# Optimization experiments

Hardware: AMD Instinct MI355X
Metric: run time of the kernel (lower is better)

## Reference

```python
import jax, jax.numpy as jnp
import numpy as np

C = 64
OUT_Z = 32
HW = 128
NUM_HEADS = 4
COMP = 16          # max(c//reduction, num_heads) = 64//4
HEAD_DIM = COMP // NUM_HEADS
MAX_Z = 32
GROWTH = 16
NEG_SLOPE = 0.2


def setup_inputs() -> dict:
    key = jax.random.key(0)
    ks = jax.random.split(key, 16)
    ch = OUT_Z * C  # 2048

    def nrm(k, shape, std):
        return (jax.random.normal(k, shape, jnp.float32) * std).astype(jnp.float32)

    inp = {
        "trans_feature": jax.random.normal(ks[0], (1, ch, HW, HW), jnp.float32),
        "ln_w": jnp.ones((C,), jnp.float32),
        "ln_b": jnp.zeros((C,), jnp.float32),
        "wq": nrm(ks[1], (C, COMP), 0.05), "bq": jnp.zeros((COMP,), jnp.float32),
        "wk": nrm(ks[2], (C, COMP), 0.05), "bk": jnp.zeros((COMP,), jnp.float32),
        "wv": nrm(ks[3], (C, COMP), 0.05), "bv": jnp.zeros((COMP,), jnp.float32),
        "wo": nrm(ks[4], (COMP, C), 0.05), "bo": jnp.zeros((C,), jnp.float32),
        "rel_z_bias": nrm(ks[5], (NUM_HEADS, 2 * MAX_Z + 1), 0.02),
        "attn_gamma": jnp.asarray(0.1, jnp.float32),
        "dw0": nrm(ks[6], (ch + 0 * GROWTH, GROWTH), 0.02), "db0": jnp.zeros((GROWTH,), jnp.float32),
        "dw1": nrm(ks[7], (ch + 1 * GROWTH, GROWTH), 0.02), "db1": jnp.zeros((GROWTH,), jnp.float32),
        "dw2": nrm(ks[8], (ch + 2 * GROWTH, GROWTH), 0.02), "db2": jnp.zeros((GROWTH,), jnp.float32),
        "fuse_w": nrm(ks[9], (ch + 3 * GROWTH, ch), 0.02), "fuse_b": jnp.zeros((ch,), jnp.float32),
        "rdc_scale": jnp.asarray(0.1, jnp.float32),
        "out_z": OUT_Z,
    }
    return inp


def _conv1x1(x, w, b):
    # 1x1 conv == per-pixel dense: x [B,Cin,H,W], w [Cin,Cout]
    return jnp.einsum('bchw,co->bohw', x, w) + b[None, :, None, None]


def _lrelu(x):
    return jnp.where(x >= 0, x, NEG_SLOPE * x)


def reference(trans_feature, ln_w, ln_b, wq, bq, wk, bk, wv, bv, wo, bo,
              rel_z_bias, attn_gamma, dw0, db0, dw1, db1, dw2, db2,
              fuse_w, fuse_b, rdc_scale, out_z):
    B, Ct, H, W = trans_feature.shape
    c = Ct // out_z
    # ---- ZAxisAttention on slices [out_z, c, H, W] ----
    x = trans_feature.reshape(out_z, c, H, W)
    xf = x.transpose(0, 2, 3, 1).reshape(out_z, H * W, c)   # [Z, N, c]
    mu = xf.mean(-1, keepdims=True)
    var = ((xf - mu) ** 2).mean(-1, keepdims=True)
    normed = (xf - mu) * jax.lax.rsqrt(var + 1e-5) * ln_w + ln_b
    pooled = normed.mean(1)                                  # [Z, c]
    q = (pooled @ wq + bq).reshape(out_z, NUM_HEADS, HEAD_DIM).transpose(1, 0, 2)
    k = (pooled @ wk + bk).reshape(out_z, NUM_HEADS, HEAD_DIM).transpose(1, 0, 2)
    v = (pooled @ wv + bv).reshape(out_z, NUM_HEADS, HEAD_DIM).transpose(1, 0, 2)
    attn = jnp.einsum('hid,hjd->hij', q, k) * (HEAD_DIM ** -0.5)  # [h, Z, Z]
    zr = jnp.arange(out_z)
    rel_idx = jnp.clip(zr[None, :] - zr[:, None] + MAX_Z, 0, 2 * MAX_Z)
    attn = jax.nn.softmax(attn + rel_z_bias[:, rel_idx], axis=-1)
    o = jnp.einsum('hij,hjd->hid', attn, v).transpose(1, 0, 2).reshape(out_z, COMP)
    o = o @ wo + bo                                          # [Z, c]
    x_z = (x + attn_gamma * o[:, :, None, None]).reshape(B, Ct, H, W)
    # ---- ResidualDenseBlock on full [B, Ct, H, W] (out_z == max_out_z) ----
    feats = trans_feature
    f0 = _lrelu(_conv1x1(feats, dw0, db0))
    feats = jnp.concatenate([feats, f0], axis=1)
    f1 = _lrelu(_conv1x1(feats, dw1, db1))
    feats = jnp.concatenate([feats, f1], axis=1)
    f2 = _lrelu(_conv1x1(feats, dw2, db2))
    feats = jnp.concatenate([feats, f2], axis=1)
    fused = _lrelu(_conv1x1(feats, fuse_w, fuse_b))
    x_rdc = trans_feature + rdc_scale * fused
    return x_z + x_rdc - trans_feature
```

## Files before the change

kernel.cpp:

```cpp
#include <hip/hip_runtime.h>
#include <hip/hip_fp8.h>

typedef unsigned char u8;
typedef unsigned short u16;
typedef long lng2 __attribute__((ext_vector_type(2)));
typedef float f32x4 __attribute__((ext_vector_type(4)));
typedef u16 u16x8 __attribute__((ext_vector_type(8)));
typedef u8 u8x16 __attribute__((ext_vector_type(16)));

#define HW_N 16384
#define NCH  2048

__device__ __forceinline__ u16 f2bf(float f) {
  union { float f; unsigned u; } v; v.f = f;
  unsigned r = v.u + 0x7FFFu + ((v.u >> 16) & 1u);
  return (u16)(r >> 16);
}
__device__ __forceinline__ float bf2f(u16 u) {
  union { unsigned u; float f; } v; v.u = ((unsigned)u) << 16; return v.f;
}
__device__ __forceinline__ u8 f2fp8(float f) {
  __hip_fp8_e4m3 t(f);
  return (u8)t.__x;
}
__device__ __forceinline__ float lrelu(float v) { return v >= 0.0f ? v : 0.2f * v; }

__device__ __forceinline__ void gload_lds16(const u8* g, u8* l) {
  __builtin_amdgcn_global_load_lds((const __attribute__((address_space(1))) void*)g,
                                   (__attribute__((address_space(3))) void*)l, 16, 0, 0);
}

__global__ __launch_bounds__(256) void k_stats(const float* __restrict__ trans,
                                               u8* __restrict__ A8,
                                               float* __restrict__ pooled_sum) {
  const int z = blockIdx.x;
  const int tid = threadIdx.x;
  const int ptile = blockIdx.y;
  const int p = ptile * 256 + tid;
  const float* src = trans + (size_t)z * 64 * HW_N + p;
  float x[64];
#pragma unroll
  for (int c = 0; c < 64; ++c) x[c] = src[(size_t)c * HW_N];
  float sum = 0.f, sq = 0.f;
#pragma unroll
  for (int c = 0; c < 64; ++c) { sum += x[c]; sq += x[c] * x[c]; }
  const float mu = sum * (1.0f / 64.0f);
  const float var = sq * (1.0f / 64.0f) - mu * mu;
  const float rstd = rsqrtf(var + 1e-5f);

  __shared__ __align__(16) u8 rawt[256 * 64];
  __shared__ __align__(16) u16 normt[256 * 64];
  const int r3m = tid & 3, r7 = tid & 7;
#pragma unroll
  for (int c = 0; c < 4; ++c) {
    u8x16 y;
#pragma unroll
    for (int w = 0; w < 16; ++w) {
      const int k = (w < 8) ? (c * 8 + w) : (32 + c * 8 + (w - 8));
      y[w] = f2fp8(x[k]);
    }
    *(u8x16*)&rawt[tid * 64 + ((c ^ r3m) << 4)] = y;
  }
#pragma unroll
  for (int c8 = 0; c8 < 8; ++c8) {
    u16x8 wn;
#pragma unroll
    for (int e = 0; e < 8; ++e) wn[e] = f2bf((x[c8 * 8 + e] - mu) * rstd);
    *(u16x8*)&normt[tid * 64 + ((c8 ^ r7) << 3)] = wn;
  }
  __syncthreads();

  u8* gbase = A8 + ((size_t)z * HW_N + (size_t)ptile * 256) * 64;
#pragma unroll
  for (int it = 0; it < 4; ++it) {
    const int o = it * 256 + tid;
    const int row = o >> 2, c4 = o & 3;
    *(u8x16*)(gbase + o * 16) = *(const u8x16*)&rawt[row * 64 + ((c4 ^ (row & 3)) << 4)];
  }

  const int c = tid & 63, q = tid >> 6;
  const int kc2 = c >> 3, e2 = c & 7;
  float s = 0.f;
#pragma unroll 8
  for (int i = 0; i < 64; ++i) {
    const int row = q * 64 + i;
    s += bf2f(normt[row * 64 + ((kc2 ^ (row & 7)) << 3) + e2]);
  }
  __shared__ float red2[4][64];
  red2[q][c] = s;
  __syncthreads();
  if (tid < 64) {
    atomicAdd(&pooled_sum[z * 64 + tid],
              red2[0][tid] + red2[1][tid] + red2[2][tid] + red2[3][tid]);
  }
}

__global__ __launch_bounds__(256) void k_wdense(const float* __restrict__ dw0,
                                                const float* __restrict__ dw1,
                                                const float* __restrict__ dw2,
                                                u8* __restrict__ Wd8) {
  const int kc = blockIdx.x;
  __shared__ float tile[64][49];
  for (int idx = threadIdx.x; idx < 3072; idx += 256) {
    const int kk = idx / 48, j = idx % 48;
    const int k = kc * 64 + kk;
    float v = (j < 16) ? dw0[k * 16 + j]
            : (j < 32) ? dw1[k * 16 + (j - 16)]
                       : dw2[k * 16 + (j - 32)];
    tile[kk][j] = v;
  }
  __syncthreads();
  for (int idx = threadIdx.x; idx < 3072; idx += 256) {
    const int j = idx / 64, kk = idx % 64;
    const int pos = ((kk >> 3) & 3) * 16 + (kk & 7) + ((kk >> 5) << 3);
    Wd8[((size_t)kc * 48 + j) * 64 + pos] = f2fp8(16.0f * tile[kk][j]);
  }
}

__global__ __launch_bounds__(256) void k_dgemm(const u8* __restrict__ A8,
                                               const u8* __restrict__ Wd8,
                                               float* __restrict__ G_part) {
  __shared__ __align__(16) u8 lsA[128 * 64];
  __shared__ __align__(16) u8 lsW[48 * 64];
  const int tid = threadIdx.x;
  const int lane = tid & 63;
  const int wave = __builtin_amdgcn_readfirstlane(tid >> 6);
  const int mb = blockIdx.x;
  const int ks = blockIdx.y;
  const int r16 = lane & 15, kgrp = lane >> 4;
  const int sgoff8 = ((lane >> 2) << 6) + (((lane & 3) ^ ((lane >> 3) & 3)) << 4);
  const int kx = (kgrp ^ ((r16 >> 1) & 3)) << 4;
  f32x4 acc[3][2] = {};

  for (int t = 0; t < 16; ++t) {
    const int kc = ks * 16 + t;
    const u8* slabA = A8 + ((size_t)kc * HW_N + (size_t)mb * 128) * 64;
    const u8* slabW = Wd8 + (size_t)kc * 48 * 64;
#pragma unroll
    for (int p = 0; p < 2; ++p)
      gload_lds16(slabA + (p * 4 + wave) * 1024 + sgoff8, lsA + (p * 4 + wave) * 1024);
    if (wave < 3)
      gload_lds16(slabW + wave * 1024 + sgoff8, lsW + wave * 1024);
    asm volatile("s_waitcnt vmcnt(0)" ::: "memory");
    __syncthreads();

    lng2 wf[3], af[2];
#pragma unroll
    for (int f = 0; f < 3; ++f)
      wf[f] = *(const lng2*)(lsW + (f * 16 + r16) * 64 + kx);
#pragma unroll
    for (int g = 0; g < 2; ++g)
      af[g] = *(const lng2*)(lsA + (wave * 32 + g * 16 + r16) * 64 + kx);
#pragma unroll
    for (int f = 0; f < 3; ++f)
#pragma unroll
      for (int g = 0; g < 2; ++g) {
        acc[f][g] = __builtin_amdgcn_mfma_f32_16x16x32_fp8_fp8(wf[f][0], af[g][0], acc[f][g], 0, 0, 0);
        acc[f][g] = __builtin_amdgcn_mfma_f32_16x16x32_fp8_fp8(wf[f][1], af[g][1], acc[f][g], 0, 0, 0);
      }
    __syncthreads();
  }

  const int rg = lane >> 4;
  float* gp = G_part + (size_t)ks * 48 * HW_N;
#pragma unroll
  for (int f = 0; f < 3; ++f)
#pragma unroll
    for (int r = 0; r < 4; ++r) {
      const int j = f * 16 + rg * 4 + r;
#pragma unroll
      for (int g = 0; g < 2; ++g) {
        const int pix = mb * 128 + wave * 32 + g * 16 + r16;
        gp[(size_t)j * HW_N + pix] = acc[f][g][r] * 0.0625f;
      }
    }
}

__global__ __launch_bounds__(256) void k_dfin(const float* __restrict__ G_part,
    const float* __restrict__ dw1, const float* __restrict__ dw2,
    const float* __restrict__ db0, const float* __restrict__ db1,
    const float* __restrict__ db2, u8* __restrict__ A8) {
  const int tid = threadIdx.x;
  const int pix = blockIdx.x * 256 + tid;
  __shared__ float w1t[16][16];
  __shared__ float w2t[32][16];
  __shared__ float biases[48];
  if (tid < 256) w1t[tid >> 4][tid & 15] = dw1[(2048 + (tid >> 4)) * 16 + (tid & 15)];
  for (int idx = tid; idx < 512; idx += 256)
    w2t[idx >> 4][idx & 15] = dw2[(2048 + (idx >> 4)) * 16 + (idx & 15)];
  if (tid < 48) biases[tid] = (tid < 16) ? db0[tid] : (tid < 32) ? db1[tid - 16] : db2[tid - 32];
  __syncthreads();

  float g[48];
#pragma unroll
  for (int j = 0; j < 48; ++j)
    g[j] = G_part[(size_t)j * HW_N + pix] + G_part[(size_t)(48 + j) * HW_N + pix];

  float f0[16], f1[16], f2[16];
#pragma unroll
  for (int j = 0; j < 16; ++j) f0[j] = lrelu(g[j] + biases[j]);
#pragma unroll
  for (int j = 0; j < 16; ++j) {
    float a = g[16 + j] + biases[16 + j];
#pragma unroll
    for (int i = 0; i < 16; ++i) a += f0[i] * w1t[i][j];
    f1[j] = lrelu(a);
  }
#pragma unroll
  for (int j = 0; j < 16; ++j) {
    float a = g[32 + j] + biases[32 + j];
#pragma unroll
    for (int i = 0; i < 16; ++i) a += f0[i] * w2t[i][j];
#pragma unroll
    for (int i = 0; i < 16; ++i) a += f1[i] * w2t[16 + i][j];
    f2[j] = lrelu(a);
  }
  u8* dst = A8 + ((size_t)32 * HW_N + pix) * 64;
#pragma unroll
  for (int c = 0; c < 4; ++c) {
    u8x16 y;
#pragma unroll
    for (int w = 0; w < 16; ++w) {
      const int k = (w < 8) ? (c * 8 + w) : (32 + c * 8 + (w - 8));
      const float v = (k < 16) ? f0[k] : (k < 32) ? f1[k - 16] : (k < 48) ? f2[k - 32] : 0.0f;
      y[w] = f2fp8(v);
    }
    *(u8x16*)(dst + c * 16) = y;
  }
}

__global__ __launch_bounds__(256) void k_attn(const float* __restrict__ pooled_sum,
    const float* __restrict__ ln_w, const float* __restrict__ ln_b,
    const float* __restrict__ wq, const float* __restrict__ bq,
    const float* __restrict__ wk, const float* __restrict__ bk,
    const float* __restrict__ wv, const float* __restrict__ bv,
    const float* __restrict__ wo, const float* __restrict__ bo,
    const float* __restrict__ relz, const float* __restrict__ attn_gamma,
    float* __restrict__ o_scaled) {
  __shared__ float pooled[2048];
  __shared__ float q[512], k[512], v[512], att[4096], tz[512];
  const int tid = threadIdx.x;
  for (int i = tid; i < 2048; i += 256) {
    int c = i & 63;
    pooled[i] = ln_w[c] * pooled_sum[i] * (1.0f / 16384.0f) + ln_b[c];
  }
  __syncthreads();
  for (int i = tid; i < 512; i += 256) {
    int z = i >> 4, e = i & 15;
    float aq = bq[e], ak = bk[e], av = bv[e];
    for (int c = 0; c < 64; ++c) {
      float p = pooled[z * 64 + c];
      aq += p * wq[c * 16 + e]; ak += p * wk[c * 16 + e]; av += p * wv[c * 16 + e];
    }
    q[i] = aq; k[i] = ak; v[i] = av;
  }
  __syncthreads();
  if (tid < 128) {
    int h = tid >> 5, zi = tid & 31;
    float s[32]; float mx = -1e30f;
#pragma unroll
    for (int j = 0; j < 32; ++j) {
      float d = 0.f;
#pragma unroll
      for (int e = 0; e < 4; ++e) d += q[zi * 16 + h * 4 + e] * k[j * 16 + h * 4 + e];
      d = d * 0.5f + relz[h * 65 + (j - zi + 32)];
      s[j] = d; mx = fmaxf(mx, d);
    }
    float ssum = 0.f;
#pragma unroll
    for (int j = 0; j < 32; ++j) { s[j] = __expf(s[j] - mx); ssum += s[j]; }
    float inv = 1.0f / ssum;
#pragma unroll
    for (int j = 0; j < 32; ++j) att[(h * 32 + zi) * 32 + j] = s[j] * inv;
  }
  __syncthreads();
  for (int i = tid; i < 512; i += 256) {
    int z = i >> 4, hd = i & 15, h = hd >> 2;
    float a = 0.f;
    for (int j = 0; j < 32; ++j) a += att[(h * 32 + z) * 32 + j] * v[j * 16 + hd];
    tz[i] = a;
  }
  __syncthreads();
  const float gamma = attn_gamma[0];
  for (int i = tid; i < 2048; i += 256) {
    int z = i >> 6, c = i & 63;
    float a = bo[c];
    for (int hd = 0; hd < 16; ++hd) a += tz[z * 16 + hd] * wo[hd * 64 + c];
    o_scaled[i] = gamma * a;
  }
}

__global__ __launch_bounds__(256) void k_wconv(const float* __restrict__ fw,
                                               u8* __restrict__ W8) {
  const int ktile = blockIdx.x;
  const int ntile = blockIdx.y;
  __shared__ float tile[64][65];
  const int tid = threadIdx.x;
  {
    const int kk0 = tid >> 6, nn = tid & 63;
#pragma unroll
    for (int it = 0; it < 16; ++it) {
      int kk = it * 4 + kk0;
      int kg = ktile * 64 + kk;
      tile[kk][nn] = (kg < 2096) ? fw[(size_t)kg * NCH + ntile * 64 + nn] : 0.0f;
    }
  }
  __syncthreads();
  {
    const int kk = tid & 63, nn0 = tid >> 6;
    const int pos = ((kk >> 3) & 3) * 16 + (kk & 7) + ((kk >> 5) << 3);
#pragma unroll
    for (int it = 0; it < 16; ++it) {
      int n = it * 4 + nn0;
      W8[((size_t)ktile * NCH + ntile * 64 + n) * 64 + pos] = f2fp8(16.0f * tile[kk][n]);
    }
  }
}

__global__ __launch_bounds__(512, 2) void k_gemm(
    const u8* __restrict__ A8, const u8* __restrict__ W8,
    const float* __restrict__ trans, const float* __restrict__ o_scaled,
    const float* __restrict__ fuse_b, const float* __restrict__ rdc_scale,
    float* __restrict__ out) {
  __shared__ __align__(16) u8 ls[65536];
  const int tid = threadIdx.x;
  const int lane = tid & 63;
  const int wave = __builtin_amdgcn_readfirstlane(tid >> 6);
  const int bid = blockIdx.x;
  const int nb = bid & 7;
  const int mb = bid >> 3;
  const int mbase = mb * 256, nbase = nb * 256;
  const int wm = wave & 1;
  const int wn = wave >> 1;
  const int wnh = wn >> 1;
  const int wrow = (wn & 1) * 64;
  const int r16 = lane & 15, kgrp = lane >> 4;
  const int sgoff8 = ((lane >> 2) << 6) + (((lane & 3) ^ ((lane >> 3) & 3)) << 4);
  const int kx = (kgrp ^ ((r16 >> 1) & 3)) << 4;

#define LA(b, h) (ls + (b) * 32768 + (h) * 8192)
#define LW(b, h) (ls + (b) * 32768 + 16384 + (h) * 8192)
#define AHALF(t, h) (A8 + ((size_t)(t) * HW_N + mbase + (h) * 128) * 64)
#define WHALF(t, h) (W8 + ((size_t)(t) * NCH + nbase + (h) * 128) * 64)
#define STAGE(rows, ldsh) gload_lds16((rows) + wave * 1024 + sgoff8, (ldsh) + wave * 1024)
#define RD8(base, row) (*(const lng2*)((base) + (row) * 64 + kx))
#define MF8(a, b, c) __builtin_amdgcn_mfma_f32_16x16x32_fp8_fp8((a), (b), (c), 0, 0, 0)

  f32x4 acc[4][8] = {};
  lng2 wf0a[2], afLa[4];
  lng2 wf0b[2], afLb[4];

  STAGE(WHALF(0, 0), LW(0, 0));
  STAGE(WHALF(0, 1), LW(0, 1));
  STAGE(AHALF(0, 0), LA(0, 0));
  STAGE(AHALF(0, 1), LA(0, 1));
  asm volatile("s_waitcnt vmcnt(0)" ::: "memory");
  __builtin_amdgcn_s_barrier();
  {
    const u8* lw0 = LW(0, wnh);
    const u8* la0 = LA(0, wm);
#pragma unroll
    for (int f = 0; f < 2; ++f) wf0a[f] = RD8(lw0, wrow + f * 16 + r16);
#pragma unroll
    for (int g = 0; g < 4; ++g) afLa[g] = RD8(la0, g * 16 + r16);
  }

#define GBODY(T, W0C, ALC, W0N, ALN)                                           \
  {                                                                            \
    const int t = (T);                                                         \
    const int buf = t & 1, nbf = buf ^ 1;                                      \
    const int tn = (t + 1 < 33) ? t + 1 : 32;                                  \
    const u8* la = LA(buf, wm);                                                \
    const u8* lw = LW(buf, wnh);                                               \
    lng2 wf1[2], afH[4];                                                       \
                            \
    _Pragma("unroll") for (int f = 0; f < 2; ++f)                              \
      wf1[f] = RD8(lw, wrow + 32 + f * 16 + r16);                              \
    STAGE(WHALF(tn, 0), LW(nbf, 0));                                           \
    STAGE(WHALF(tn, 1), LW(nbf, 1));                                           \
    __builtin_amdgcn_s_setprio(1);                                             \
    _Pragma("unroll") for (int f = 0; f < 2; ++f)                              \
      _Pragma("unroll") for (int g = 0; g < 4; ++g) {                          \
        acc[f][g] = MF8(W0C[f][0], ALC[g][0], acc[f][g]);                      \
        acc[f][g] = MF8(W0C[f][1], ALC[g][1], acc[f][g]);                      \
      }                                                                        \
    __builtin_amdgcn_s_setprio(0);                                             \
                            \
    _Pragma("unroll") for (int g = 0; g < 4; ++g)                              \
      afH[g] = RD8(la, 64 + g * 16 + r16);                                     \
    STAGE(AHALF(tn, 0), LA(nbf, 0));                                           \
    STAGE(AHALF(tn, 1), LA(nbf, 1));                                           \
    __builtin_amdgcn_s_setprio(1);                                             \
    _Pragma("unroll") for (int f = 0; f < 2; ++f)                              \
      _Pragma("unroll") for (int g = 0; g < 4; ++g) {                          \
        acc[2 + f][g] = MF8(wf1[f][0], ALC[g][0], acc[2 + f][g]);              \
        acc[2 + f][g] = MF8(wf1[f][1], ALC[g][1], acc[2 + f][g]);              \
      }                                                                        \
    __builtin_amdgcn_s_setprio(0);                                             \
                                            \
    __builtin_amdgcn_s_setprio(1);                                             \
    _Pragma("unroll") for (int f = 0; f < 2; ++f)                              \
      _Pragma("unroll") for (int g = 0; g < 4; ++g) {                          \
        acc[2 + f][4 + g] = MF8(wf1[f][0], afH[g][0], acc[2 + f][4 + g]);      \
        acc[2 + f][4 + g] = MF8(wf1[f][1], afH[g][1], acc[2 + f][4 + g]);      \
      }                                                                        \
    __builtin_amdgcn_s_setprio(0);                                             \
            \
    asm volatile("s_waitcnt vmcnt(0)" ::: "memory");                           \
    __builtin_amdgcn_s_barrier();                                              \
    {                                                                          \
      const u8* lan = LA(nbf, wm);                                             \
      const u8* lwn = LW(nbf, wnh);                                            \
      _Pragma("unroll") for (int f = 0; f < 2; ++f)                            \
        W0N[f] = RD8(lwn, wrow + f * 16 + r16);                                \
      _Pragma("unroll") for (int g = 0; g < 4; ++g)                            \
        ALN[g] = RD8(lan, g * 16 + r16);                                       \
    }                                                                          \
    __builtin_amdgcn_s_setprio(1);                                             \
    _Pragma("unroll") for (int f = 0; f < 2; ++f)                              \
      _Pragma("unroll") for (int g = 0; g < 4; ++g) {                          \
        acc[f][4 + g] = MF8(W0C[f][0], afH[g][0], acc[f][4 + g]);              \
        acc[f][4 + g] = MF8(W0C[f][1], afH[g][1], acc[f][4 + g]);              \
      }                                                                        \
    __builtin_amdgcn_s_setprio(0);                                             \
  }

  for (int u = 0; u < 16; ++u) {
    GBODY(2 * u, wf0a, afLa, wf0b, afLb);
    GBODY(2 * u + 1, wf0b, afLb, wf0a, afLa);
  }
  GBODY(32, wf0a, afLa, wf0b, afLb);

  asm volatile("s_waitcnt vmcnt(0)" ::: "memory");

  const float rdc = rdc_scale[0];
  const int rg = lane >> 4;
#pragma unroll
  for (int f = 0; f < 4; ++f) {
#pragma unroll
    for (int r = 0; r < 4; ++r) {
      const int row = nbase + wn * 64 + f * 16 + rg * 4 + r;
      const float ob = o_scaled[row], fb = fuse_b[row];
#pragma unroll
      for (int g = 0; g < 8; ++g) {
        const int col = mbase + wm * 128 + g * 16 + r16;
        float v = lrelu(acc[f][g][r] * 0.0625f + fb);
        const size_t idx = (size_t)row * HW_N + col;
        out[idx] = trans[idx] + rdc * v + ob;
      }
    }
  }
#undef GBODY
#undef LA
#undef LW
#undef AHALF
#undef WHALF
#undef STAGE
#undef RD8
#undef MF8
}

extern "C" void kernel_launch(void* const* d_in, const int* in_sizes, int n_in,
                              void* d_out, int out_size, void* d_ws, size_t ws_size,
                              hipStream_t stream) {
  (void)in_sizes; (void)n_in; (void)out_size; (void)ws_size;
  const float* trans = (const float*)d_in[0];
  const float* ln_w  = (const float*)d_in[1];
  const float* ln_b  = (const float*)d_in[2];
  const float* wq = (const float*)d_in[3];  const float* bq = (const float*)d_in[4];
  const float* wk = (const float*)d_in[5];  const float* bk = (const float*)d_in[6];
  const float* wv = (const float*)d_in[7];  const float* bv = (const float*)d_in[8];
  const float* wo = (const float*)d_in[9];  const float* bo = (const float*)d_in[10];
  const float* relz  = (const float*)d_in[11];
  const float* gamma = (const float*)d_in[12];
  const float* dw0 = (const float*)d_in[13]; const float* db0 = (const float*)d_in[14];
  const float* dw1 = (const float*)d_in[15]; const float* db1 = (const float*)d_in[16];
  const float* dw2 = (const float*)d_in[17]; const float* db2 = (const float*)d_in[18];
  const float* fuse_w = (const float*)d_in[19];
  const float* fuse_b = (const float*)d_in[20];
  const float* rdc    = (const float*)d_in[21];
  float* out = (float*)d_out;

  char* ws = (char*)d_ws;
  u8*    A8         = (u8*)ws;
  float* G_part     = (float*)(ws + 34603008);
  u8*    Wd8        = (u8*)(ws + 34603008 + 6291456);
  u8*    W8         = (u8*)(ws + 34603008);
  float* pooled_sum = (float*)(ws + 40992768);
  float* o_scaled   = (float*)(ws + 41000960);

  hipMemsetAsync(pooled_sum, 0, 2048 * sizeof(float), stream);
  k_stats<<<dim3(32, 64), 256, 0, stream>>>(trans, A8, pooled_sum);
  k_wdense<<<dim3(32), 256, 0, stream>>>(dw0, dw1, dw2, Wd8);
  k_dgemm<<<dim3(128, 2), 256, 0, stream>>>(A8, Wd8, G_part);
  k_dfin<<<dim3(64), 256, 0, stream>>>(G_part, dw1, dw2, db0, db1, db2, A8);
  k_attn<<<dim3(1), 256, 0, stream>>>(pooled_sum, ln_w, ln_b, wq, bq, wk, bk, wv, bv,
                                      wo, bo, relz, gamma, o_scaled);
  k_wconv<<<dim3(33, 32), 256, 0, stream>>>(fuse_w, W8);
  k_gemm<<<dim3(512), 512, 0, stream>>>(A8, W8, trans, o_scaled, fuse_b, rdc, out);
}
```

Measured before the change: 218.0 us.

## Switch FP8 GEMMs to 16x16x128 scaled MFMA with two-slab K staging

Replaces the 16x16x32 fp8 MFMA pairs with the MI355X 16x16x128 f8f6f4 scaled MFMA (unit scales) in both the dense-block GEMM and the main fuse GEMM. The K-slab interleave permutation is dropped so each 64-wide slab is stored linearly, and two consecutive slabs are staged per iteration into doubled LDS (128KB in the main GEMM), halving loop trip counts and MFMA instruction count. Zero padding is added for the odd slab count via memsets of an extra A8/W8 slab, and workspace offsets shift. The larger LDS footprint limits occupancy to one block per CU, and the restructured pipeline changes how loads overlap with compute.

```diff
diff --git a/kernel.cpp b/kernel.cpp
--- a/kernel.cpp
+++ b/kernel.cpp
@@ -3,7 +3,8 @@
 
 typedef unsigned char u8;
 typedef unsigned short u16;
-typedef long lng2 __attribute__((ext_vector_type(2)));
+typedef int i32x4 __attribute__((ext_vector_type(4)));
+typedef int i32x8 __attribute__((ext_vector_type(8)));
 typedef float f32x4 __attribute__((ext_vector_type(4)));
 typedef u16 u16x8 __attribute__((ext_vector_type(8)));
 typedef u8 u8x16 __attribute__((ext_vector_type(16)));
@@ -30,6 +31,9 @@
                                    (__attribute__((address_space(3))) void*)l, 16, 0, 0);
 }
 
+#define MFS(a, b, c) \
+  __builtin_amdgcn_mfma_scale_f32_16x16x128_f8f6f4((a), (b), (c), 0, 0, 0, 0x7F7F7F7F, 0, 0x7F7F7F7F)
+
 __global__ __launch_bounds__(256) void k_stats(const float* __restrict__ trans,
                                                u8* __restrict__ A8,
                                                float* __restrict__ pooled_sum) {
@@ -55,10 +59,7 @@
   for (int c = 0; c < 4; ++c) {
     u8x16 y;
 #pragma unroll
-    for (int w = 0; w < 16; ++w) {
-      const int k = (w < 8) ? (c * 8 + w) : (32 + c * 8 + (w - 8));
-      y[w] = f2fp8(x[k]);
-    }
+    for (int w = 0; w < 16; ++w) y[w] = f2fp8(x[c * 16 + w]);
     *(u8x16*)&rawt[tid * 64 + ((c ^ r3m) << 4)] = y;
   }
 #pragma unroll
@@ -112,54 +113,63 @@
   __syncthreads();
   for (int idx = threadIdx.x; idx < 3072; idx += 256) {
     const int j = idx / 64, kk = idx % 64;
-    const int pos = ((kk >> 3) & 3) * 16 + (kk & 7) + ((kk >> 5) << 3);
-    Wd8[((size_t)kc * 48 + j) * 64 + pos] = f2fp8(16.0f * tile[kk][j]);
+    Wd8[((size_t)kc * 48 + j) * 64 + kk] = f2fp8(16.0f * tile[kk][j]);
   }
 }
 
 __global__ __launch_bounds__(256) void k_dgemm(const u8* __restrict__ A8,
                                                const u8* __restrict__ Wd8,
                                                float* __restrict__ G_part) {
-  __shared__ __align__(16) u8 lsA[128 * 64];
-  __shared__ __align__(16) u8 lsW[48 * 64];
+  __shared__ __align__(16) u8 lsA[16384];
+  __shared__ __align__(16) u8 lsW[8192];
   const int tid = threadIdx.x;
   const int lane = tid & 63;
   const int wave = __builtin_amdgcn_readfirstlane(tid >> 6);
   const int mb = blockIdx.x;
   const int ks = blockIdx.y;
-  const int r16 = lane & 15, kgrp = lane >> 4;
+  const int r16 = lane & 15, kg = lane >> 4;
+  const int h2 = (kg & 1) << 1, sreg = kg >> 1;
   const int sgoff8 = ((lane >> 2) << 6) + (((lane & 3) ^ ((lane >> 3) & 3)) << 4);
-  const int kx = (kgrp ^ ((r16 >> 1) & 3)) << 4;
   f32x4 acc[3][2] = {};
 
-  for (int t = 0; t < 16; ++t) {
-    const int kc = ks * 16 + t;
-    const u8* slabA = A8 + ((size_t)kc * HW_N + (size_t)mb * 128) * 64;
-    const u8* slabW = Wd8 + (size_t)kc * 48 * 64;
-#pragma unroll
-    for (int p = 0; p < 2; ++p)
-      gload_lds16(slabA + (p * 4 + wave) * 1024 + sgoff8, lsA + (p * 4 + wave) * 1024);
-    if (wave < 3)
-      gload_lds16(slabW + wave * 1024 + sgoff8, lsW + wave * 1024);
+#define RDFD(R, STR, row, out)                                                  \
+  {                                                                             \
+    const int off0_ = sreg * (STR) + ((row) << 6) + ((h2 ^ (((row) >> 1) & 3)) << 4); \
+    i32x4 lo_ = *(const i32x4*)((R) + off0_);                                   \
+    i32x4 hi_ = *(const i32x4*)((R) + (off0_ ^ 16));                            \
+    out = __builtin_shufflevector(lo_, hi_, 0, 1, 2, 3, 4, 5, 6, 7);            \
+  }
+
+  for (int t = 0; t < 8; ++t) {
+    const int kc0 = ks * 16 + 2 * t;
+    const u8* srcA0 = A8 + ((size_t)kc0 * HW_N + (size_t)mb * 128) * 64;
+    const u8* srcA1 = srcA0 + (size_t)HW_N * 64;
+    const u8* srcW0 = Wd8 + (size_t)kc0 * 3072;
+    const u8* srcW1 = srcW0 + 3072;
+    gload_lds16(srcA0 + wave * 2048 + sgoff8, lsA + wave * 2048);
+    gload_lds16(srcA0 + wave * 2048 + 1024 + sgoff8, lsA + wave * 2048 + 1024);
+    gload_lds16(srcA1 + wave * 2048 + sgoff8, lsA + 8192 + wave * 2048);
+    gload_lds16(srcA1 + wave * 2048 + 1024 + sgoff8, lsA + 8192 + wave * 2048 + 1024);
+    if (wave < 3) {
+      gload_lds16(srcW0 + wave * 1024 + sgoff8, lsW + wave * 1024);
+      gload_lds16(srcW1 + wave * 1024 + sgoff8, lsW + 4096 + wave * 1024);
+    }
     asm volatile("s_waitcnt vmcnt(0)" ::: "memory");
     __syncthreads();
 
-    lng2 wf[3], af[2];
+    i32x8 wf[3], af[2];
+#pragma unroll
+    for (int f = 0; f < 3; ++f) RDFD(lsW, 4096, f * 16 + r16, wf[f]);
+#pragma unroll
+    for (int g = 0; g < 2; ++g) RDFD(lsA, 8192, wave * 32 + g * 16 + r16, af[g]);
 #pragma unroll
     for (int f = 0; f < 3; ++f)
-      wf[f] = *(const lng2*)(lsW + (f * 16 + r16) * 64 + kx);
-#pragma unroll
-    for (int g = 0; g < 2; ++g)
-      af[g] = *(const lng2*)(lsA + (wave * 32 + g * 16 + r16) * 64 + kx);
-#pragma unroll
-    for (int f = 0; f < 3; ++f)
-#pragma unroll
-      for (int g = 0; g < 2; ++g) {
-        acc[f][g] = __builtin_amdgcn_mfma_f32_16x16x32_fp8_fp8(wf[f][0], af[g][0], acc[f][g], 0, 0, 0);
-        acc[f][g] = __builtin_amdgcn_mfma_f32_16x16x32_fp8_fp8(wf[f][1], af[g][1], acc[f][g], 0, 0, 0);
-      }
+#pragma unroll
+      for (int g = 0; g < 2; ++g)
+        acc[f][g] = MFS(wf[f], af[g], acc[f][g]);
     __syncthreads();
   }
+#undef RDFD
 
   const int rg = lane >> 4;
   float* gp = G_part + (size_t)ks * 48 * HW_N;
@@ -221,7 +231,7 @@
     u8x16 y;
 #pragma unroll
     for (int w = 0; w < 16; ++w) {
-      const int k = (w < 8) ? (c * 8 + w) : (32 + c * 8 + (w - 8));
+      const int k = c * 16 + w;
       const float v = (k < 16) ? f0[k] : (k < 32) ? f1[k - 16] : (k < 48) ? f2[k - 32] : 0.0f;
       y[w] = f2fp8(v);
     }
@@ -301,18 +311,17 @@
 #pragma unroll
     for (int it = 0; it < 16; ++it) {
       int kk = it * 4 + kk0;
-      int kg = ktile * 64 + kk;
-      tile[kk][nn] = (kg < 2096) ? fw[(size_t)kg * NCH + ntile * 64 + nn] : 0.0f;
+      int kg2 = ktile * 64 + kk;
+      tile[kk][nn] = (kg2 < 2096) ? fw[(size_t)kg2 * NCH + ntile * 64 + nn] : 0.0f;
     }
   }
   __syncthreads();
   {
     const int kk = tid & 63, nn0 = tid >> 6;
-    const int pos = ((kk >> 3) & 3) * 16 + (kk & 7) + ((kk >> 5) << 3);
 #pragma unroll
     for (int it = 0; it < 16; ++it) {
       int n = it * 4 + nn0;
-      W8[((size_t)ktile * NCH + ntile * 64 + n) * 64 + pos] = f2fp8(16.0f * tile[kk][n]);
+      W8[((size_t)ktile * NCH + ntile * 64 + n) * 64 + kk] = f2fp8(16.0f * tile[kk][n]);
     }
   }
 }
@@ -322,7 +331,7 @@
     const float* __restrict__ trans, const float* __restrict__ o_scaled,
     const float* __restrict__ fuse_b, const float* __restrict__ rdc_scale,
     float* __restrict__ out) {
-  __shared__ __align__(16) u8 ls[65536];
+  __shared__ __align__(16) u8 ls[131072];
   const int tid = threadIdx.x;
   const int lane = tid & 63;
   const int wave = __builtin_amdgcn_readfirstlane(tid >> 6);
@@ -332,104 +341,90 @@
   const int mbase = mb * 256, nbase = nb * 256;
   const int wm = wave & 1;
   const int wn = wave >> 1;
-  const int wnh = wn >> 1;
-  const int wrow = (wn & 1) * 64;
-  const int r16 = lane & 15, kgrp = lane >> 4;
+  const int r16 = lane & 15, kg = lane >> 4;
+  const int h2 = (kg & 1) << 1, sreg = kg >> 1;
   const int sgoff8 = ((lane >> 2) << 6) + (((lane & 3) ^ ((lane >> 3) & 3)) << 4);
-  const int kx = (kgrp ^ ((r16 >> 1) & 3)) << 4;
-
-#define LA(b, h) (ls + (b) * 32768 + (h) * 8192)
-#define LW(b, h) (ls + (b) * 32768 + 16384 + (h) * 8192)
-#define AHALF(t, h) (A8 + ((size_t)(t) * HW_N + mbase + (h) * 128) * 64)
-#define WHALF(t, h) (W8 + ((size_t)(t) * NCH + nbase + (h) * 128) * 64)
-#define STAGE(rows, ldsh) gload_lds16((rows) + wave * 1024 + sgoff8, (ldsh) + wave * 1024)
-#define RD8(base, row) (*(const lng2*)((base) + (row) * 64 + kx))
-#define MF8(a, b, c) __builtin_amdgcn_mfma_f32_16x16x32_fp8_fp8((a), (b), (c), 0, 0, 0)
+
+#define LAR(b) (ls + (b) * 65536)
+#define LWR(b) (ls + (b) * 65536 + 32768)
+#define ASLAB(s2) (A8 + ((size_t)(s2) * HW_N + mbase) * 64)
+#define WSLAB(s2) (W8 + ((size_t)(s2) * NCH + nbase) * 64)
+#define STAGE16(src, dst)                                                      \
+  do {                                                                         \
+    gload_lds16((src) + wave * 2048 + sgoff8, (dst) + wave * 2048);            \
+    gload_lds16((src) + wave * 2048 + 1024 + sgoff8, (dst) + wave * 2048 + 1024); \
+  } while (0)
+#define RDF(R, row, outv)                                                      \
+  {                                                                            \
+    const int off0_ = (sreg << 14) + ((row) << 6) + ((h2 ^ (((row) >> 1) & 3)) << 4); \
+    i32x4 lo_ = *(const i32x4*)((R) + off0_);                                  \
+    i32x4 hi_ = *(const i32x4*)((R) + (off0_ ^ 16));                           \
+    outv = __builtin_shufflevector(lo_, hi_, 0, 1, 2, 3, 4, 5, 6, 7);          \
+  }
 
   f32x4 acc[4][8] = {};
-  lng2 wf0a[2], afLa[4];
-  lng2 wf0b[2], afLb[4];
-
-  STAGE(WHALF(0, 0), LW(0, 0));
-  STAGE(WHALF(0, 1), LW(0, 1));
-  STAGE(AHALF(0, 0), LA(0, 0));
-  STAGE(AHALF(0, 1), LA(0, 1));
+  i32x8 wf0a[2], wf0b[2];
+
+  STAGE16(WSLAB(0), LWR(0));
+  STAGE16(WSLAB(1), LWR(0) + 16384);
+  STAGE16(ASLAB(0), LAR(0));
+  STAGE16(ASLAB(1), LAR(0) + 16384);
   asm volatile("s_waitcnt vmcnt(0)" ::: "memory");
   __builtin_amdgcn_s_barrier();
-  {
-    const u8* lw0 = LW(0, wnh);
-    const u8* la0 = LA(0, wm);
-#pragma unroll
-    for (int f = 0; f < 2; ++f) wf0a[f] = RD8(lw0, wrow + f * 16 + r16);
-#pragma unroll
-    for (int g = 0; g < 4; ++g) afLa[g] = RD8(la0, g * 16 + r16);
-  }
-
-#define GBODY(T, W0C, ALC, W0N, ALN)                                           \
+#pragma unroll
+  for (int f = 0; f < 2; ++f) RDF(LWR(0), wn * 64 + f * 16 + r16, wf0a[f]);
+
+#define GB(T, W0C, W0N)                                                        \
   {                                                                            \
-    const int t = (T);                                                         \
-    const int buf = t & 1, nbf = buf ^ 1;                                      \
-    const int tn = (t + 1 < 33) ? t + 1 : 32;                                  \
-    const u8* la = LA(buf, wm);                                                \
-    const u8* lw = LW(buf, wnh);                                               \
-    lng2 wf1[2], afH[4];                                                       \
-                            \
-    _Pragma("unroll") for (int f = 0; f < 2; ++f)                              \
-      wf1[f] = RD8(lw, wrow + 32 + f * 16 + r16);                              \
-    STAGE(WHALF(tn, 0), LW(nbf, 0));                                           \
-    STAGE(WHALF(tn, 1), LW(nbf, 1));                                           \
+    const int t_ = (T);                                                        \
+    const int b_ = t_ & 1, nb_ = b_ ^ 1;                                       \
+    const int tn_ = (t_ + 1 < 17) ? t_ + 1 : 16;                               \
+    const u8* Ab_ = LAR(b_);                                                   \
+    const u8* Wb_ = LWR(b_);                                                   \
+    i32x8 afL[4], afH[4], wf1[2];                                              \
+                               \
+    _Pragma("unroll") for (int g = 0; g < 4; ++g)                              \
+      RDF(Ab_, wm * 128 + g * 16 + r16, afL[g]);                               \
+    STAGE16(WSLAB(2 * tn_), LWR(nb_));                                         \
+    STAGE16(WSLAB(2 * tn_ + 1), LWR(nb_) + 16384);                             \
     __builtin_amdgcn_s_setprio(1);                                             \
     _Pragma("unroll") for (int f = 0; f < 2; ++f)                              \
-      _Pragma("unroll") for (int g = 0; g < 4; ++g) {                          \
-        acc[f][g] = MF8(W0C[f][0], ALC[g][0], acc[f][g]);                      \
-        acc[f][g] = MF8(W0C[f][1], ALC[g][1], acc[f][g]);                      \
-      }                                                                        \
+      _Pragma("unroll") for (int g = 0; g < 4; ++g)                            \
+        acc[f][g] = MFS(W0C[f], afL[g], acc[f][g]);                            \
     __builtin_amdgcn_s_setprio(0);                                             \
-                            \
+                               \
     _Pragma("unroll") for (int g = 0; g < 4; ++g)                              \
-      afH[g] = RD8(la, 64 + g * 16 + r16);                                     \
-    STAGE(AHALF(tn, 0), LA(nbf, 0));                                           \
-    STAGE(AHALF(tn, 1), LA(nbf, 1));                                           \
+      RDF(Ab_, wm * 128 + 64 + g * 16 + r16, afH[g]);                          \
+    STAGE16(ASLAB(2 * tn_), LAR(nb_));                                         \
+    STAGE16(ASLAB(2 * tn_ + 1), LAR(nb_) + 16384);                             \
     __builtin_amdgcn_s_setprio(1);                                             \
     _Pragma("unroll") for (int f = 0; f < 2; ++f)                              \
-      _Pragma("unroll") for (int g = 0; g < 4; ++g) {                          \
-        acc[2 + f][g] = MF8(wf1[f][0], ALC[g][0], acc[2 + f][g]);              \
-        acc[2 + f][g] = MF8(wf1[f][1], ALC[g][1], acc[2 + f][g]);              \
-      }                                                                        \
+      _Pragma("unroll") for (int g = 0; g < 4; ++g)                            \
+        acc[f][4 + g] = MFS(W0C[f], afH[g], acc[f][4 + g]);                    \
     __builtin_amdgcn_s_setprio(0);                                             \
-                                            \
+                                  \
+    _Pragma("unroll") for (int f = 0; f < 2; ++f)                              \
+      RDF(Wb_, wn * 64 + 32 + f * 16 + r16, wf1[f]);                           \
     __builtin_amdgcn_s_setprio(1);                                             \
     _Pragma("unroll") for (int f = 0; f < 2; ++f)                              \
-      _Pragma("unroll") for (int g = 0; g < 4; ++g) {                          \
-        acc[2 + f][4 + g] = MF8(wf1[f][0], afH[g][0], acc[2 + f][4 + g]);      \
-        acc[2 + f][4 + g] = MF8(wf1[f][1], afH[g][1], acc[2 + f][4 + g]);      \
-      }                                                                        \
+      _Pragma("unroll") for (int g = 0; g < 4; ++g)                            \
+        acc[2 + f][g] = MFS(wf1[f], afL[g], acc[2 + f][g]);                    \
+    _Pragma("unroll") for (int f = 0; f < 2; ++f)                              \
+      _Pragma("unroll") for (int g = 0; g < 4; ++g)                            \
+        acc[2 + f][4 + g] = MFS(wf1[f], afH[g], acc[2 + f][4 + g]);            \
     __builtin_amdgcn_s_setprio(0);                                             \
-            \
+                                   \
     asm volatile("s_waitcnt vmcnt(0)" ::: "memory");                           \
     __builtin_amdgcn_s_barrier();                                              \
-    {                                                                          \
-      const u8* lan = LA(nbf, wm);                                             \
-      const u8* lwn = LW(nbf, wnh);                                            \
-      _Pragma("unroll") for (int f = 0; f < 2; ++f)                            \
-        W0N[f] = RD8(lwn, wrow + f * 16 + r16);                                \
-      _Pragma("unroll") for (int g = 0; g < 4; ++g)                            \
-        ALN[g] = RD8(lan, g * 16 + r16);                                       \
-    }                                                                          \
-    __builtin_amdgcn_s_setprio(1);                                             \
-    _Pragma("unroll") for (int f = 0; f < 2; ++f)                              \
-      _Pragma("unroll") for (int g = 0; g < 4; ++g) {                          \
-        acc[f][4 + g] = MF8(W0C[f][0], afH[g][0], acc[f][4 + g]);              \
-        acc[f][4 + g] = MF8(W0C[f][1], afH[g][1], acc[f][4 + g]);              \
-      }                                                                        \
-    __builtin_amdgcn_s_setprio(0);                                             \
-  }
-
-  for (int u = 0; u < 16; ++u) {
-    GBODY(2 * u, wf0a, afLa, wf0b, afLb);
-    GBODY(2 * u + 1, wf0b, afLb, wf0a, afLa);
-  }
-  GBODY(32, wf0a, afLa, wf0b, afLb);
+    _Pragma("unroll") for (int f = 0; f < 2; ++f)                              \
+      RDF(LWR(nb_), wn * 64 + f * 16 + r16, W0N[f]);                           \
+  }
+
+  for (int u = 0; u < 8; ++u) {
+    GB(2 * u, wf0a, wf0b);
+    GB(2 * u + 1, wf0b, wf0a);
+  }
+  GB(16, wf0a, wf0b);
 
   asm volatile("s_waitcnt vmcnt(0)" ::: "memory");
 
@@ -450,14 +445,13 @@
       }
     }
   }
-#undef GBODY
-#undef LA
-#undef LW
-#undef AHALF
-#undef WHALF
-#undef STAGE
-#undef RD8
-#undef MF8
+#undef GB
+#undef RDF
+#undef STAGE16
+#undef LAR
+#undef LWR
+#undef ASLAB
+#undef WSLAB
 }
 
 extern "C" void kernel_launch(void* const* d_in, const int* in_sizes, int n_in,
@@ -483,17 +477,19 @@
 
   char* ws = (char*)d_ws;
   u8*    A8         = (u8*)ws;
-  float* G_part     = (float*)(ws + 34603008);
-  u8*    Wd8        = (u8*)(ws + 34603008 + 6291456);
-  u8*    W8         = (u8*)(ws + 34603008);
-  float* pooled_sum = (float*)(ws + 40992768);
-  float* o_scaled   = (float*)(ws + 41000960);
+  float* G_part     = (float*)(ws + 35651584);
+  u8*    Wd8        = (u8*)(ws + 35651584 + 6291456);
+  u8*    W8         = (u8*)(ws + 35651584);
+  float* pooled_sum = (float*)(ws + 42041344);
+  float* o_scaled   = (float*)(ws + 42049536);
 
   hipMemsetAsync(pooled_sum, 0, 2048 * sizeof(float), stream);
+  hipMemsetAsync(A8 + (size_t)33 * HW_N * 64, 0, (size_t)HW_N * 64, stream);
   k_stats<<<dim3(32, 64), 256, 0, stream>>>(trans, A8, pooled_sum);
   k_wdense<<<dim3(32), 256, 0, stream>>>(dw0, dw1, dw2, Wd8);
   k_dgemm<<<dim3(128, 2), 256, 0, stream>>>(A8, Wd8, G_part);
   k_dfin<<<dim3(64), 256, 0, stream>>>(G_part, dw1, dw2, db0, db1, db2, A8);
+  hipMemsetAsync(W8 + (size_t)33 * NCH * 64, 0, (size_t)NCH * 64, stream);
   k_attn<<<dim3(1), 256, 0, stream>>>(pooled_sum, ln_w, ln_b, wq, bq, wk, bk, wv, bv,
                                       wo, bo, relz, gamma, o_scaled);
   k_wconv<<<dim3(33, 32), 256, 0, stream>>>(fuse_w, W8);
```

Measured after the change: 279.6 us. 1.28x slower.

## Fuse dense GEMM with finalize and merge weight-packing kernels

Applied to the files above, without the earlier changes.

Merges the fuse-weight and dense-weight fp8 packing kernels into one launch with an extra grid row. The dense GEMM no longer splits K across two blocks. Each block now runs all 32 K-chunks and finishes the three small lrelu dense layers in-kernel through an LDS transpose, which drops the G_part round trip through global memory and two kernel launches. The cost is that the dense GEMM grid shrinks from 256 to 128 blocks with twice the serial K loop, and only half the threads do the finalize step.

```diff
diff --git a/kernel.cpp b/kernel.cpp
--- a/kernel.cpp
+++ b/kernel.cpp
@@ -95,47 +95,85 @@
   }
 }
 
-__global__ __launch_bounds__(256) void k_wdense(const float* __restrict__ dw0,
-                                                const float* __restrict__ dw1,
-                                                const float* __restrict__ dw2,
-                                                u8* __restrict__ Wd8) {
-  const int kc = blockIdx.x;
-  __shared__ float tile[64][49];
-  for (int idx = threadIdx.x; idx < 3072; idx += 256) {
-    const int kk = idx / 48, j = idx % 48;
-    const int k = kc * 64 + kk;
-    float v = (j < 16) ? dw0[k * 16 + j]
-            : (j < 32) ? dw1[k * 16 + (j - 16)]
-                       : dw2[k * 16 + (j - 32)];
-    tile[kk][j] = v;
-  }
-  __syncthreads();
-  for (int idx = threadIdx.x; idx < 3072; idx += 256) {
-    const int j = idx / 64, kk = idx % 64;
+__global__ __launch_bounds__(256) void k_wpack(const float* __restrict__ fw,
+                                               const float* __restrict__ dw0,
+                                               const float* __restrict__ dw1,
+                                               const float* __restrict__ dw2,
+                                               u8* __restrict__ W8,
+                                               u8* __restrict__ Wd8) {
+  __shared__ float tile[64][65];
+  const int tid = threadIdx.x;
+  const int ktile = blockIdx.x;
+  const int yb = blockIdx.y;
+  if (yb == 32) {
+    const int kc = ktile;
+    if (kc >= 32) return;
+    for (int idx = tid; idx < 3072; idx += 256) {
+      const int kk = idx / 48, j = idx % 48;
+      const int k = kc * 64 + kk;
+      float v = (j < 16) ? dw0[k * 16 + j]
+              : (j < 32) ? dw1[k * 16 + (j - 16)]
+                         : dw2[k * 16 + (j - 32)];
+      tile[kk][j] = v;
+    }
+    __syncthreads();
+    for (int idx = tid; idx < 3072; idx += 256) {
+      const int j = idx / 64, kk = idx % 64;
+      const int pos = ((kk >> 3) & 3) * 16 + (kk & 7) + ((kk >> 5) << 3);
+      Wd8[((size_t)kc * 48 + j) * 64 + pos] = f2fp8(16.0f * tile[kk][j]);
+    }
+    return;
+  }
+  const int ntile = yb;
+  {
+    const int kk0 = tid >> 6, nn = tid & 63;
+#pragma unroll
+    for (int it = 0; it < 16; ++it) {
+      int kk = it * 4 + kk0;
+      int kg = ktile * 64 + kk;
+      tile[kk][nn] = (kg < 2096) ? fw[(size_t)kg * NCH + ntile * 64 + nn] : 0.0f;
+    }
+  }
+  __syncthreads();
+  {
+    const int kk = tid & 63, nn0 = tid >> 6;
     const int pos = ((kk >> 3) & 3) * 16 + (kk & 7) + ((kk >> 5) << 3);
-    Wd8[((size_t)kc * 48 + j) * 64 + pos] = f2fp8(16.0f * tile[kk][j]);
-  }
-}
-
-__global__ __launch_bounds__(256) void k_dgemm(const u8* __restrict__ A8,
-                                               const u8* __restrict__ Wd8,
-                                               float* __restrict__ G_part) {
+#pragma unroll
+    for (int it = 0; it < 16; ++it) {
+      int n = it * 4 + nn0;
+      W8[((size_t)ktile * NCH + ntile * 64 + n) * 64 + pos] = f2fp8(16.0f * tile[kk][n]);
+    }
+  }
+}
+
+__global__ __launch_bounds__(256) void k_dense(const u8* __restrict__ A8,
+    const u8* __restrict__ Wd8,
+    const float* __restrict__ dw1, const float* __restrict__ dw2,
+    const float* __restrict__ db0, const float* __restrict__ db1,
+    const float* __restrict__ db2, u8* __restrict__ A8out) {
   __shared__ __align__(16) u8 lsA[128 * 64];
   __shared__ __align__(16) u8 lsW[48 * 64];
+  __shared__ float trn[128][49];
+  __shared__ float w1t[16][16];
+  __shared__ float w2t[32][16];
+  __shared__ float biases[48];
   const int tid = threadIdx.x;
   const int lane = tid & 63;
   const int wave = __builtin_amdgcn_readfirstlane(tid >> 6);
   const int mb = blockIdx.x;
-  const int ks = blockIdx.y;
   const int r16 = lane & 15, kgrp = lane >> 4;
   const int sgoff8 = ((lane >> 2) << 6) + (((lane & 3) ^ ((lane >> 3) & 3)) << 4);
   const int kx = (kgrp ^ ((r16 >> 1) & 3)) << 4;
+
+  if (tid < 256) w1t[tid >> 4][tid & 15] = dw1[(2048 + (tid >> 4)) * 16 + (tid & 15)];
+  for (int idx = tid; idx < 512; idx += 256)
+    w2t[idx >> 4][idx & 15] = dw2[(2048 + (idx >> 4)) * 16 + (idx & 15)];
+  if (tid < 48) biases[tid] = (tid < 16) ? db0[tid] : (tid < 32) ? db1[tid - 16] : db2[tid - 32];
+
   f32x4 acc[3][2] = {};
-
-  for (int t = 0; t < 16; ++t) {
-    const int kc = ks * 16 + t;
-    const u8* slabA = A8 + ((size_t)kc * HW_N + (size_t)mb * 128) * 64;
-    const u8* slabW = Wd8 + (size_t)kc * 48 * 64;
+  for (int t = 0; t < 32; ++t) {
+    const u8* slabA = A8 + ((size_t)t * HW_N + (size_t)mb * 128) * 64;
+    const u8* slabW = Wd8 + (size_t)t * 48 * 64;
 #pragma unroll
     for (int p = 0; p < 2; ++p)
       gload_lds16(slabA + (p * 4 + wave) * 1024 + sgoff8, lsA + (p * 4 + wave) * 1024);
@@ -162,70 +200,50 @@
   }
 
   const int rg = lane >> 4;
-  float* gp = G_part + (size_t)ks * 48 * HW_N;
 #pragma unroll
   for (int f = 0; f < 3; ++f)
 #pragma unroll
-    for (int r = 0; r < 4; ++r) {
-      const int j = f * 16 + rg * 4 + r;
-#pragma unroll
-      for (int g = 0; g < 2; ++g) {
-        const int pix = mb * 128 + wave * 32 + g * 16 + r16;
-        gp[(size_t)j * HW_N + pix] = acc[f][g][r] * 0.0625f;
+    for (int r = 0; r < 4; ++r)
+#pragma unroll
+      for (int g = 0; g < 2; ++g)
+        trn[wave * 32 + g * 16 + r16][f * 16 + rg * 4 + r] = acc[f][g][r] * 0.0625f;
+  __syncthreads();
+
+  if (tid < 128) {
+    float gv[48];
+#pragma unroll
+    for (int j = 0; j < 48; ++j) gv[j] = trn[tid][j];
+    float f0[16], f1[16], f2[16];
+#pragma unroll
+    for (int j = 0; j < 16; ++j) f0[j] = lrelu(gv[j] + biases[j]);
+#pragma unroll
+    for (int j = 0; j < 16; ++j) {
+      float a = gv[16 + j] + biases[16 + j];
+#pragma unroll
+      for (int i = 0; i < 16; ++i) a += f0[i] * w1t[i][j];
+      f1[j] = lrelu(a);
+    }
+#pragma unroll
+    for (int j = 0; j < 16; ++j) {
+      float a = gv[32 + j] + biases[32 + j];
+#pragma unroll
+      for (int i = 0; i < 16; ++i) a += f0[i] * w2t[i][j];
+#pragma unroll
+      for (int i = 0; i < 16; ++i) a += f1[i] * w2t[16 + i][j];
+      f2[j] = lrelu(a);
+    }
+    u8* dst = A8out + ((size_t)32 * HW_N + mb * 128 + tid) * 64;
+#pragma unroll
+    for (int c = 0; c < 4; ++c) {
+      u8x16 y;
+#pragma unroll
+      for (int w = 0; w < 16; ++w) {
+        const int k = (w < 8) ? (c * 8 + w) : (32 + c * 8 + (w - 8));
+        const float v = (k < 16) ? f0[k] : (k < 32) ? f1[k - 16] : (k < 48) ? f2[k - 32] : 0.0f;
+        y[w] = f2fp8(v);
       }
-    }
-}
-
-__global__ __launch_bounds__(256) void k_dfin(const float* __restrict__ G_part,
-    const float* __restrict__ dw1, const float* __restrict__ dw2,
-    const float* __restrict__ db0, const float* __restrict__ db1,
-    const float* __restrict__ db2, u8* __restrict__ A8) {
-  const int tid = threadIdx.x;
-  const int pix = blockIdx.x * 256 + tid;
-  __shared__ float w1t[16][16];
-  __shared__ float w2t[32][16];
-  __shared__ float biases[48];
-  if (tid < 256) w1t[tid >> 4][tid & 15] = dw1[(2048 + (tid >> 4)) * 16 + (tid & 15)];
-  for (int idx = tid; idx < 512; idx += 256)
-    w2t[idx >> 4][idx & 15] = dw2[(2048 + (idx >> 4)) * 16 + (idx & 15)];
-  if (tid < 48) biases[tid] = (tid < 16) ? db0[tid] : (tid < 32) ? db1[tid - 16] : db2[tid - 32];
-  __syncthreads();
-
-  float g[48];
-#pragma unroll
-  for (int j = 0; j < 48; ++j)
-    g[j] = G_part[(size_t)j * HW_N + pix] + G_part[(size_t)(48 + j) * HW_N + pix];
-
-  float f0[16], f1[16], f2[16];
-#pragma unroll
-  for (int j = 0; j < 16; ++j) f0[j] = lrelu(g[j] + biases[j]);
-#pragma unroll
-  for (int j = 0; j < 16; ++j) {
-    float a = g[16 + j] + biases[16 + j];
-#pragma unroll
-    for (int i = 0; i < 16; ++i) a += f0[i] * w1t[i][j];
-    f1[j] = lrelu(a);
-  }
-#pragma unroll
-  for (int j = 0; j < 16; ++j) {
-    float a = g[32 + j] + biases[32 + j];
-#pragma unroll
-    for (int i = 0; i < 16; ++i) a += f0[i] * w2t[i][j];
-#pragma unroll
-    for (int i = 0; i < 16; ++i) a += f1[i] * w2t[16 + i][j];
-    f2[j] = lrelu(a);
-  }
-  u8* dst = A8 + ((size_t)32 * HW_N + pix) * 64;
-#pragma unroll
-  for (int c = 0; c < 4; ++c) {
-    u8x16 y;
-#pragma unroll
-    for (int w = 0; w < 16; ++w) {
-      const int k = (w < 8) ? (c * 8 + w) : (32 + c * 8 + (w - 8));
-      const float v = (k < 16) ? f0[k] : (k < 32) ? f1[k - 16] : (k < 48) ? f2[k - 32] : 0.0f;
-      y[w] = f2fp8(v);
-    }
-    *(u8x16*)(dst + c * 16) = y;
+      *(u8x16*)(dst + c * 16) = y;
+    }
   }
 }
 
@@ -287,33 +305,6 @@
     float a = bo[c];
     for (int hd = 0; hd < 16; ++hd) a += tz[z * 16 + hd] * wo[hd * 64 + c];
     o_scaled[i] = gamma * a;
-  }
-}
-
-__global__ __launch_bounds__(256) void k_wconv(const float* __restrict__ fw,
-                                               u8* __restrict__ W8) {
-  const int ktile = blockIdx.x;
-  const int ntile = blockIdx.y;
-  __shared__ float tile[64][65];
-  const int tid = threadIdx.x;
-  {
-    const int kk0 = tid >> 6, nn = tid & 63;
-#pragma unroll
-    for (int it = 0; it < 16; ++it) {
-      int kk = it * 4 + kk0;
-      int kg = ktile * 64 + kk;
-      tile[kk][nn] = (kg < 2096) ? fw[(size_t)kg * NCH + ntile * 64 + nn] : 0.0f;
-    }
-  }
-  __syncthreads();
-  {
-    const int kk = tid & 63, nn0 = tid >> 6;
-    const int pos = ((kk >> 3) & 3) * 16 + (kk & 7) + ((kk >> 5) << 3);
-#pragma unroll
-    for (int it = 0; it < 16; ++it) {
-      int n = it * 4 + nn0;
-      W8[((size_t)ktile * NCH + ntile * 64 + n) * 64 + pos] = f2fp8(16.0f * tile[kk][n]);
-    }
   }
 }
 
@@ -483,19 +474,16 @@
 
   char* ws = (char*)d_ws;
   u8*    A8         = (u8*)ws;
-  float* G_part     = (float*)(ws + 34603008);
-  u8*    Wd8        = (u8*)(ws + 34603008 + 6291456);
   u8*    W8         = (u8*)(ws + 34603008);
-  float* pooled_sum = (float*)(ws + 40992768);
-  float* o_scaled   = (float*)(ws + 41000960);
+  u8*    Wd8        = (u8*)(ws + 38928384);
+  float* pooled_sum = (float*)(ws + 39026688);
+  float* o_scaled   = (float*)(ws + 39034880);
 
   hipMemsetAsync(pooled_sum, 0, 2048 * sizeof(float), stream);
   k_stats<<<dim3(32, 64), 256, 0, stream>>>(trans, A8, pooled_sum);
-  k_wdense<<<dim3(32), 256, 0, stream>>>(dw0, dw1, dw2, Wd8);
-  k_dgemm<<<dim3(128, 2), 256, 0, stream>>>(A8, Wd8, G_part);
-  k_dfin<<<dim3(64), 256, 0, stream>>>(G_part, dw1, dw2, db0, db1, db2, A8);
+  k_wpack<<<dim3(33, 33), 256, 0, stream>>>(fuse_w, dw0, dw1, dw2, W8, Wd8);
+  k_dense<<<dim3(128), 256, 0, stream>>>(A8, Wd8, dw1, dw2, db0, db1, db2, A8);
   k_attn<<<dim3(1), 256, 0, stream>>>(pooled_sum, ln_w, ln_b, wq, bq, wk, bk, wv, bv,
                                       wo, bo, relz, gamma, o_scaled);
-  k_wconv<<<dim3(33, 32), 256, 0, stream>>>(fuse_w, W8);
   k_gemm<<<dim3(512), 512, 0, stream>>>(A8, W8, trans, o_scaled, fuse_b, rdc, out);
 }
```

Result: faster. 206.1 us, median of 2 (-5.5%).
